# Kernel tuning notes

Measured on AMD Instinct MI355X. Metric: run time of the kernel, lower is better.

## Reference

```python
import jax, jax.numpy as jnp
import numpy as np
from jax import lax

C, NORI, NROT, K, PAD = 256, 8, 2, 3, 1
B, H, W = 16, 64, 64
EPS = 1e-5


def setup_inputs() -> dict:
    key = jax.random.key(0)
    k1, k2, k3 = jax.random.split(key, 3)
    x = jax.random.normal(k1, (B, C, H, W), dtype=jnp.float32)
    # rotate_arf() output: [nRot*C, nOri*C, K, K]
    weight_all = jax.random.normal(k2, (NROT * C, NORI * C, K, K), dtype=jnp.float32) * 0.02
    bias_all = jax.random.normal(k3, (NROT * C,), dtype=jnp.float32) * 0.02
    alpha = jnp.float32(1.0)
    gamma = jnp.ones((C,), dtype=jnp.float32)
    beta = jnp.zeros((C,), dtype=jnp.float32)
    return {"x": x, "weight_all": weight_all, "bias_all": bias_all,
            "alpha": alpha, "gamma": gamma, "beta": beta}


def _forward(x, weight_all, bias_all, alpha, gamma, beta):
    # Loop of nOri*nRot convs over the same x with different weight blocks,
    # all accumulated into one [B,C,H,W] tensor == single conv with summed blocks
    # (conv is linear in the weights): fused form of the original loop.
    W_eff = weight_all.reshape(NROT, C, NORI, C, K, K).sum(axis=(0, 2))  # [C, C, K, K]
    b_eff = bias_all.reshape(NROT, C).sum(axis=0) * NORI                 # [C]
    d_sum = lax.conv_general_dilated(
        x, W_eff, window_strides=(1, 1), padding=[(PAD, PAD), (PAD, PAD)],
        dimension_numbers=("NCHW", "OIHW", "NCHW"))
    d_sum = d_sum + b_eff[None, :, None, None]
    d_mean = d_sum / float(NORI * NROT)
    out = x + alpha * d_mean
    # BatchNorm2d, training mode: biased batch stats over (B, H, W)
    mean = out.mean(axis=(0, 2, 3))
    var = ((out - mean[None, :, None, None]) ** 2).mean(axis=(0, 2, 3))
    inv = lax.rsqrt(var + EPS)
    y = (out - mean[None, :, None, None]) * (gamma * inv)[None, :, None, None] \
        + beta[None, :, None, None]
    return y


def reference(x, weight_all, bias_all, alpha, gamma, beta):
    return _forward(x, weight_all, bias_all, alpha, gamma, beta)
```

## Files before the change

### kernel.cpp

```cpp
#include <hip/hip_runtime.h>
#include <stdint.h>

typedef __attribute__((__ext_vector_type__(8))) __bf16 bf16x8;
typedef __attribute__((__ext_vector_type__(4))) float  f32x4;

#define XT_OFF    0ul
#define WT_OFF    33554432ul
#define BEFF_OFF  34734080ul
#define ZERO_OFF  34737152ul
#define STATS_OFF 34737408ul
#define V_OFF     35651584ul
#define WS_NEED   (V_OFF + 33554432ul)

__device__ inline void gload_lds16(const void* g, void* l) {
  __builtin_amdgcn_global_load_lds((const __attribute__((address_space(1))) void*)g,
                                   (__attribute__((address_space(3))) void*)l,
                                   16, 0, 0);
}

__global__ void k_wred(const float* __restrict__ w, const float* __restrict__ bias,
                       const float* __restrict__ alpha_p, __bf16* __restrict__ Wt,
                       float* __restrict__ beff, float* __restrict__ zerob,
                       float* __restrict__ statsG) {
  const int co = blockIdx.x;
  const int ci = threadIdx.x;
  float a[9];
#pragma unroll
  for (int t = 0; t < 9; ++t) a[t] = 0.f;
#pragma unroll
  for (int r = 0; r < 2; ++r)
#pragma unroll
    for (int o = 0; o < 8; ++o) {
      const float* p = w + ((size_t)(r * 256 + co) * 2048 + (size_t)(o * 256 + ci)) * 9;
#pragma unroll
      for (int t = 0; t < 9; ++t) a[t] += p[t];
    }
  const float sc = alpha_p[0] * 0.0625f;
  const int s = ci >> 6, cis = ci & 63;
#pragma unroll
  for (int t = 0; t < 9; ++t)
    Wt[(size_t)(t * 4 + s) * 16384 + co * 64 + cis] = (__bf16)(a[t] * sc);
  if (ci == 0) beff[co] = (bias[co] + bias[256 + co]) * 8.0f * sc;
  if (blockIdx.x == 0) {
    statsG[ci] = 0.f; statsG[256 + ci] = 0.f;
    if (ci < 64) zerob[ci] = 0.f;
  }
}

__global__ void k_xpose(const float* __restrict__ x, __bf16* __restrict__ xT) {
  __shared__ __bf16 lds[64 * 258];
  int bh = blockIdx.x;
  int b = bh >> 6, h = bh & 63;
  int t = threadIdx.x;
  int w = t & 63, cg = t >> 6;
  const float* xb = x + ((size_t)b * 16384 + h) * 64;
#pragma unroll 4
  for (int cb = 0; cb < 256; cb += 4) {
    int ci = cb + cg;
    lds[w * 258 + ci] = (__bf16)xb[(size_t)ci * 4096 + w];
  }
  __syncthreads();
  const uint32_t* l32 = (const uint32_t*)lds;
  uint32_t* o32 = (uint32_t*)(xT + ((size_t)b * 64 + h) * 64 * 256);
  int c2 = t & 127, wg = t >> 7;
  for (int w0 = 0; w0 < 64; w0 += 2) {
    int ww = w0 + wg;
    o32[ww * 128 + c2] = l32[ww * 129 + c2];
  }
}

#define A_BYTES 51200
#define B_BYTES 32768

__global__ __launch_bounds__(1024) void k_conv(
    const float* __restrict__ x, const __bf16* __restrict__ xT,
    const __bf16* __restrict__ Wt, const float* __restrict__ beff,
    const __bf16* __restrict__ zerob, float* __restrict__ out,
    float* __restrict__ statsG, __bf16* __restrict__ vout, int use_v16)
{
  __shared__ __align__(16) char lds[A_BYTES + 3 * B_BYTES + 2048];
  const int bb   = blockIdx.x >> 4;
  const int ho0  = (blockIdx.x & 15) << 2;
  const int tid  = threadIdx.x;
  const int lane = tid & 63;
  const int wid  = tid >> 6;
  const int wr   = wid >> 2;
  const int wc   = wid & 3;
  const int l15  = lane & 15;

  f32x4 acc[4][4];
#pragma unroll
  for (int i = 0; i < 4; ++i)
#pragma unroll
    for (int j = 0; j < 4; ++j)
#pragma unroll
      for (int r = 0; r < 4; ++r) acc[i][j][r] = 0.f;

  const char* zb = (const char*)zerob;

  int boff[4][2];
#pragma unroll
  for (int j = 0; j < 4; ++j)
#pragma unroll
    for (int kk = 0; kk < 2; ++kk) {
      const int co     = (wc << 6) + (j << 4) + l15;
      const int ci_off = (kk << 5) + ((lane >> 4) << 3);
      boff[j][kk] = ((co << 7) + (ci_off << 1)) ^ ((co & 7) << 4);
    }
  const int bl = lane >> 3;
  const int bsrcLane = (bl << 7) + (((lane & 7) ^ (bl & 7)) << 4);

  auto stageA = [&](int s) {
    const int ci0 = s << 6;
    for (int t = wid; t < 50; t += 16) {
      const int ch = (t << 3) + (lane >> 3);
      const int r  = ch / 66;
      const int c  = ch - r * 66;
      const int ir = ho0 - 1 + r;
      const int ic = c - 1;
      const int k  = (lane & 7) ^ (ch & 7);
      const char* src;
      if (ch < 396 && ir >= 0 && ir < 64 && ic >= 0 && ic < 64)
        src = (const char*)(xT + ((((size_t)bb << 6) + ir) * 64 + ic) * 256 + ci0 + (k << 3));
      else
        src = zb + (k << 4);
      gload_lds16(src, lds + (t << 10));
    }
  };

  auto stageB = [&](int ph, int bi) {
    char* buf = lds + A_BYTES + bi * B_BYTES;
    const int s2 = ph / 9, tp = ph - s2 * 9;
    const char* wsrc = (const char*)Wt + ((size_t)(tp * 4 + s2) << 15) + bsrcLane;
    gload_lds16(wsrc + (wid << 10), buf + (wid << 10));
    gload_lds16(wsrc + ((wid + 16) << 10), buf + ((wid + 16) << 10));
  };

  stageA(0);
  stageB(0, 0);
  stageB(1, 1);
  asm volatile("s_waitcnt vmcnt(0)" ::: "memory");
  __builtin_amdgcn_s_barrier();
  asm volatile("" ::: "memory");

  int s = 0, tap = 0, bcur = 0;
  for (int p = 0; p < 36; ++p) {
    if (p + 2 < 36) {
      int bnx = bcur + 2; if (bnx >= 3) bnx -= 3;
      stageB(p + 2, bnx);
    }
    const int dh = (tap >= 6) ? 2 : (tap >= 3 ? 1 : 0);
    const int dw = tap - dh * 3;
    const char* Bb = lds + A_BYTES + bcur * B_BYTES;
    __builtin_amdgcn_s_setprio(1);
#pragma unroll
    for (int kk = 0; kk < 2; ++kk) {
      const int ci_off = (kk << 5) + ((lane >> 4) << 3);
      bf16x8 av[4];
#pragma unroll
      for (int i = 0; i < 4; ++i) {
        const int pos = (wr + dh) * 66 + (i << 4) + l15 + dw;
        const int off = ((pos << 7) + (ci_off << 1)) ^ ((pos & 7) << 4);
        av[i] = *(const bf16x8*)(lds + off);
      }
#pragma unroll
      for (int j = 0; j < 4; ++j) {
        const bf16x8 bv = *(const bf16x8*)(Bb + boff[j][kk]);
#pragma unroll
        for (int i = 0; i < 4; ++i)
          acc[i][j] = __builtin_amdgcn_mfma_f32_16x16x32_bf16(av[i], bv, acc[i][j], 0, 0, 0);
      }
    }
    __builtin_amdgcn_s_setprio(0);

    if (tap == 8 && s < 3) {
      asm volatile("s_waitcnt vmcnt(0)" ::: "memory");
      __builtin_amdgcn_s_barrier();
      asm volatile("" ::: "memory");
      stageA(s + 1);
      asm volatile("s_waitcnt vmcnt(0)" ::: "memory");
      __builtin_amdgcn_s_barrier();
      asm volatile("" ::: "memory");
    } else if (p + 2 < 36) {
      asm volatile("s_waitcnt vmcnt(2)" ::: "memory");
      __builtin_amdgcn_s_barrier();
      asm volatile("" ::: "memory");
    } else if (p < 35) {
      asm volatile("s_waitcnt vmcnt(0)" ::: "memory");
      __builtin_amdgcn_s_barrier();
      asm volatile("" ::: "memory");
    }
    if (++tap == 9) { tap = 0; ++s; }
    if (++bcur == 3) bcur = 0;
  }

  __syncthreads();
  float* lstat = (float*)(lds + A_BYTES + 3 * B_BYTES);
  if (tid < 512) lstat[tid] = 0.f;
  __syncthreads();

  const int wq = lane >> 4;
  const int ho = ho0 + wr;
#pragma unroll
  for (int j = 0; j < 4; ++j) {
    const int co = (wc << 6) + (j << 4) + l15;
    const float be = beff[co];
    const size_t base = ((((size_t)bb << 8) + (size_t)co) << 12) + (ho << 6);
    float r1 = 0.f, r2 = 0.f;
#pragma unroll
    for (int i = 0; i < 4; ++i) {
      const int w0 = (i << 4) + (wq << 2);
      const float4 xv = *(const float4*)(x + base + w0);
      float4 v;
      v.x = acc[i][j][0] + xv.x + be;
      v.y = acc[i][j][1] + xv.y + be;
      v.z = acc[i][j][2] + xv.z + be;
      v.w = acc[i][j][3] + xv.w + be;
      r1 += v.x + v.y + v.z + v.w;
      r2 += v.x * v.x + v.y * v.y + v.z * v.z + v.w * v.w;
      if (use_v16) {
        union { __bf16 h[4]; uint2 u2; } pk;
        pk.h[0] = (__bf16)v.x; pk.h[1] = (__bf16)v.y;
        pk.h[2] = (__bf16)v.z; pk.h[3] = (__bf16)v.w;
        *(uint2*)(vout + base + w0) = pk.u2;
      } else {
        *(float4*)(out + base + w0) = v;
      }
    }
    r1 += __shfl_xor(r1, 16); r2 += __shfl_xor(r2, 16);
    r1 += __shfl_xor(r1, 32); r2 += __shfl_xor(r2, 32);
    if (lane < 16) {
      atomicAdd(&lstat[co], r1);
      atomicAdd(&lstat[256 + co], r2);
    }
  }
  __syncthreads();
  if (tid < 512) atomicAdd(&statsG[tid], lstat[tid]);
}

__global__ void k_apply_v16(const __bf16* __restrict__ v, float* __restrict__ out,
                            const float* __restrict__ statsG,
                            const float* __restrict__ gamma,
                            const float* __restrict__ beta) {
  __shared__ float ssc[256], ssh[256];
  const int t = threadIdx.x;
  {
    const float mean = statsG[t] * (1.f / 65536.f);
    const float var  = statsG[256 + t] * (1.f / 65536.f) - mean * mean;
    const float inv  = rsqrtf(var + 1e-5f);
    const float sc   = gamma[t] * inv;
    ssc[t] = sc;
    ssh[t] = beta[t] - mean * sc;
  }
  __syncthreads();
  const ushort4* vp = (const ushort4*)v;
  float4* op = (float4*)out;
  for (size_t g = (size_t)blockIdx.x * 256 + t; g < 4194304ul; g += (size_t)gridDim.x * 256) {
    const int co = (int)((g >> 10) & 255);
    const ushort4 pv = vp[g];
    const float sc = ssc[co], sh = ssh[co];
    float4 y;
    y.x = __uint_as_float((uint32_t)pv.x << 16) * sc + sh;
    y.y = __uint_as_float((uint32_t)pv.y << 16) * sc + sh;
    y.z = __uint_as_float((uint32_t)pv.z << 16) * sc + sh;
    y.w = __uint_as_float((uint32_t)pv.w << 16) * sc + sh;
    op[g] = y;
  }
}

__global__ void k_apply_f32(float* __restrict__ out, const float* __restrict__ statsG,
                            const float* __restrict__ gamma,
                            const float* __restrict__ beta) {
  __shared__ float ssc[256], ssh[256];
  const int t = threadIdx.x;
  {
    const float mean = statsG[t] * (1.f / 65536.f);
    const float var  = statsG[256 + t] * (1.f / 65536.f) - mean * mean;
    const float inv  = rsqrtf(var + 1e-5f);
    const float sc   = gamma[t] * inv;
    ssc[t] = sc;
    ssh[t] = beta[t] - mean * sc;
  }
  __syncthreads();
  float4* op = (float4*)out;
  for (size_t g = (size_t)blockIdx.x * 256 + t; g < 4194304ul; g += (size_t)gridDim.x * 256) {
    const int co = (int)((g >> 10) & 255);
    float4 y = op[g];
    const float sc = ssc[co], sh = ssh[co];
    y.x = y.x * sc + sh; y.y = y.y * sc + sh;
    y.z = y.z * sc + sh; y.w = y.w * sc + sh;
    op[g] = y;
  }
}

extern "C" void kernel_launch(void* const* d_in, const int* in_sizes, int n_in,
                              void* d_out, int out_size, void* d_ws, size_t ws_size,
                              hipStream_t stream) {
  const float* x     = (const float*)d_in[0];
  const float* wall  = (const float*)d_in[1];
  const float* bias  = (const float*)d_in[2];
  const float* alpha = (const float*)d_in[3];
  const float* gamma = (const float*)d_in[4];
  const float* beta  = (const float*)d_in[5];
  float* out = (float*)d_out;

  char* ws = (char*)d_ws;
  __bf16* xT     = (__bf16*)(ws + XT_OFF);
  __bf16* Wt     = (__bf16*)(ws + WT_OFF);
  float*  beff   = (float*)(ws + BEFF_OFF);
  float*  zerob  = (float*)(ws + ZERO_OFF);
  float*  statsG = (float*)(ws + STATS_OFF);
  __bf16* vbuf   = (__bf16*)(ws + V_OFF);
  const int use_v16 = (ws_size >= WS_NEED) ? 1 : 0;

  k_wred<<<256, 256, 0, stream>>>(wall, bias, alpha, Wt, beff, zerob, statsG);
  k_xpose<<<1024, 256, 0, stream>>>(x, xT);
  k_conv<<<256, 1024, 0, stream>>>(x, xT, Wt, beff, (const __bf16*)zerob, out,
                                   statsG, vbuf, use_v16);
  if (use_v16)
    k_apply_v16<<<2048, 256, 0, stream>>>(vbuf, out, statsG, gamma, beta);
  else
    k_apply_f32<<<2048, 256, 0, stream>>>(out, statsG, gamma, beta);
}
```

Baseline: 126.7 us.

## Merge prep kernels, stage bf16 conv output through LDS for wide stores

Folds the weight-reduction and input-transpose kernels into one launch, with the block index choosing the role, which saves a kernel launch and lets the two jobs run concurrently. In the conv epilogue the bf16 intermediate is written to a per-wave swizzled LDS region and read back so each lane issues 16-byte global stores instead of 8-byte ones. The apply kernel now reads 16-byte vectors of eight bf16 values. This adds LDS traffic and waitcnt stalls in the epilogue, and the stats buffer is moved to offset 32768, which relies on the earlier LDS contents no longer being needed.

```diff
diff --git a/kernel.cpp b/kernel.cpp
--- a/kernel.cpp
+++ b/kernel.cpp
@@ -18,54 +18,55 @@
                                    16, 0, 0);
 }
 
-__global__ void k_wred(const float* __restrict__ w, const float* __restrict__ bias,
+__global__ void k_prep(const float* __restrict__ w, const float* __restrict__ bias,
                        const float* __restrict__ alpha_p, __bf16* __restrict__ Wt,
                        float* __restrict__ beff, float* __restrict__ zerob,
-                       float* __restrict__ statsG) {
-  const int co = blockIdx.x;
-  const int ci = threadIdx.x;
-  float a[9];
-#pragma unroll
-  for (int t = 0; t < 9; ++t) a[t] = 0.f;
-#pragma unroll
-  for (int r = 0; r < 2; ++r)
-#pragma unroll
-    for (int o = 0; o < 8; ++o) {
-      const float* p = w + ((size_t)(r * 256 + co) * 2048 + (size_t)(o * 256 + ci)) * 9;
-#pragma unroll
-      for (int t = 0; t < 9; ++t) a[t] += p[t];
-    }
-  const float sc = alpha_p[0] * 0.0625f;
-  const int s = ci >> 6, cis = ci & 63;
-#pragma unroll
-  for (int t = 0; t < 9; ++t)
-    Wt[(size_t)(t * 4 + s) * 16384 + co * 64 + cis] = (__bf16)(a[t] * sc);
-  if (ci == 0) beff[co] = (bias[co] + bias[256 + co]) * 8.0f * sc;
-  if (blockIdx.x == 0) {
-    statsG[ci] = 0.f; statsG[256 + ci] = 0.f;
-    if (ci < 64) zerob[ci] = 0.f;
-  }
-}
-
-__global__ void k_xpose(const float* __restrict__ x, __bf16* __restrict__ xT) {
+                       float* __restrict__ statsG,
+                       const float* __restrict__ x, __bf16* __restrict__ xT) {
   __shared__ __bf16 lds[64 * 258];
-  int bh = blockIdx.x;
-  int b = bh >> 6, h = bh & 63;
-  int t = threadIdx.x;
-  int w = t & 63, cg = t >> 6;
-  const float* xb = x + ((size_t)b * 16384 + h) * 64;
+  if (blockIdx.x < 256) {
+    const int co = blockIdx.x;
+    const int ci = threadIdx.x;
+    float a[9];
+#pragma unroll
+    for (int t = 0; t < 9; ++t) a[t] = 0.f;
+#pragma unroll
+    for (int r = 0; r < 2; ++r)
+#pragma unroll
+      for (int o = 0; o < 8; ++o) {
+        const float* p = w + ((size_t)(r * 256 + co) * 2048 + (size_t)(o * 256 + ci)) * 9;
+#pragma unroll
+        for (int t = 0; t < 9; ++t) a[t] += p[t];
+      }
+    const float sc = alpha_p[0] * 0.0625f;
+    const int s = ci >> 6, cis = ci & 63;
+#pragma unroll
+    for (int t = 0; t < 9; ++t)
+      Wt[(size_t)(t * 4 + s) * 16384 + co * 64 + cis] = (__bf16)(a[t] * sc);
+    if (ci == 0) beff[co] = (bias[co] + bias[256 + co]) * 8.0f * sc;
+    if (blockIdx.x == 0) {
+      statsG[ci] = 0.f; statsG[256 + ci] = 0.f;
+      if (ci < 64) zerob[ci] = 0.f;
+    }
+  } else {
+    int bh = blockIdx.x - 256;
+    int b = bh >> 6, h = bh & 63;
+    int t = threadIdx.x;
+    int w2 = t & 63, cg = t >> 6;
+    const float* xb = x + ((size_t)b * 16384 + h) * 64;
 #pragma unroll 4
-  for (int cb = 0; cb < 256; cb += 4) {
-    int ci = cb + cg;
-    lds[w * 258 + ci] = (__bf16)xb[(size_t)ci * 4096 + w];
-  }
-  __syncthreads();
-  const uint32_t* l32 = (const uint32_t*)lds;
-  uint32_t* o32 = (uint32_t*)(xT + ((size_t)b * 64 + h) * 64 * 256);
-  int c2 = t & 127, wg = t >> 7;
-  for (int w0 = 0; w0 < 64; w0 += 2) {
-    int ww = w0 + wg;
-    o32[ww * 128 + c2] = l32[ww * 129 + c2];
+    for (int cb = 0; cb < 256; cb += 4) {
+      int ci = cb + cg;
+      lds[w2 * 258 + ci] = (__bf16)xb[(size_t)ci * 4096 + w2];
+    }
+    __syncthreads();
+    const uint32_t* l32 = (const uint32_t*)lds;
+    uint32_t* o32 = (uint32_t*)(xT + ((size_t)b * 64 + h) * 64 * 256);
+    int c2 = t & 127, wg = t >> 7;
+    for (int w0 = 0; w0 < 64; w0 += 2) {
+      int ww = w0 + wg;
+      o32[ww * 128 + c2] = l32[ww * 129 + c2];
+    }
   }
 }
 
@@ -195,12 +196,14 @@
   }
 
   __syncthreads();
-  float* lstat = (float*)(lds + A_BYTES + 3 * B_BYTES);
+  float* lstat = (float*)(lds + 32768);
   if (tid < 512) lstat[tid] = 0.f;
   __syncthreads();
 
+  char* wreg = lds + wid * 2048;
   const int wq = lane >> 4;
   const int ho = ho0 + wr;
+  const int xorco = (l15 & 7) << 4;
 #pragma unroll
   for (int j = 0; j < 4; ++j) {
     const int co = (wc << 6) + (j << 4) + l15;
@@ -219,10 +222,11 @@
       r1 += v.x + v.y + v.z + v.w;
       r2 += v.x * v.x + v.y * v.y + v.z * v.z + v.w * v.w;
       if (use_v16) {
-        union { __bf16 h[4]; uint2 u2; } pk;
+        union { __bf16 h[4]; uint64_t u; } pk;
         pk.h[0] = (__bf16)v.x; pk.h[1] = (__bf16)v.y;
         pk.h[2] = (__bf16)v.z; pk.h[3] = (__bf16)v.w;
-        *(uint2*)(vout + base + w0) = pk.u2;
+        const int wa = (l15 << 7) + (i << 5) + (wq << 3);
+        *(uint64_t*)(wreg + (wa ^ xorco)) = pk.u;
       } else {
         *(float4*)(out + base + w0) = v;
       }
@@ -232,6 +236,20 @@
     if (lane < 16) {
       atomicAdd(&lstat[co], r1);
       atomicAdd(&lstat[256 + co], r2);
+    }
+    if (use_v16) {
+      asm volatile("s_waitcnt lgkmcnt(0)" ::: "memory");
+#pragma unroll
+      for (int t2 = 0; t2 < 2; ++t2) {
+        const int co_r = lane >> 2;
+        const int ch   = (lane & 3) + (t2 << 2);
+        const int ra   = (co_r << 7) + (ch << 4);
+        const uint4 pv = *(const uint4*)(wreg + (ra ^ ((co_r & 7) << 4)));
+        const int co_g = (wc << 6) + (j << 4) + co_r;
+        const size_t oi = ((((size_t)bb << 8) + (size_t)co_g) << 12) + (ho << 6) + (ch << 3);
+        *(uint4*)(vout + oi) = pv;
+      }
+      asm volatile("s_waitcnt lgkmcnt(0)" ::: "memory");
     }
   }
   __syncthreads();
@@ -253,18 +271,23 @@
     ssh[t] = beta[t] - mean * sc;
   }
   __syncthreads();
-  const ushort4* vp = (const ushort4*)v;
-  float4* op = (float4*)out;
-  for (size_t g = (size_t)blockIdx.x * 256 + t; g < 4194304ul; g += (size_t)gridDim.x * 256) {
-    const int co = (int)((g >> 10) & 255);
-    const ushort4 pv = vp[g];
+  const uint4* vp = (const uint4*)v;
+  for (size_t g = (size_t)blockIdx.x * 256 + t; g < 2097152ul; g += (size_t)gridDim.x * 256) {
+    const int co = (int)((g >> 9) & 255);
+    const uint4 pv = vp[g];
     const float sc = ssc[co], sh = ssh[co];
-    float4 y;
-    y.x = __uint_as_float((uint32_t)pv.x << 16) * sc + sh;
-    y.y = __uint_as_float((uint32_t)pv.y << 16) * sc + sh;
-    y.z = __uint_as_float((uint32_t)pv.z << 16) * sc + sh;
-    y.w = __uint_as_float((uint32_t)pv.w << 16) * sc + sh;
-    op[g] = y;
+    float4 y0, y1;
+    y0.x = __uint_as_float((pv.x & 0xffffu) << 16) * sc + sh;
+    y0.y = __uint_as_float(pv.x & 0xffff0000u) * sc + sh;
+    y0.z = __uint_as_float((pv.y & 0xffffu) << 16) * sc + sh;
+    y0.w = __uint_as_float(pv.y & 0xffff0000u) * sc + sh;
+    y1.x = __uint_as_float((pv.z & 0xffffu) << 16) * sc + sh;
+    y1.y = __uint_as_float(pv.z & 0xffff0000u) * sc + sh;
+    y1.z = __uint_as_float((pv.w & 0xffffu) << 16) * sc + sh;
+    y1.w = __uint_as_float(pv.w & 0xffff0000u) * sc + sh;
+    float4* op = (float4*)(out + g * 8);
+    op[0] = y0;
+    op[1] = y1;
   }
 }
 
@@ -313,8 +336,7 @@
   __bf16* vbuf   = (__bf16*)(ws + V_OFF);
   const int use_v16 = (ws_size >= WS_NEED) ? 1 : 0;
 
-  k_wred<<<256, 256, 0, stream>>>(wall, bias, alpha, Wt, beff, zerob, statsG);
-  k_xpose<<<1024, 256, 0, stream>>>(x, xT);
+  k_prep<<<1280, 256, 0, stream>>>(wall, bias, alpha, Wt, beff, zerob, statsG, x, xT);
   k_conv<<<256, 1024, 0, stream>>>(x, xT, Wt, beff, (const __bf16*)zerob, out,
                                    statsG, vbuf, use_v16);
   if (use_v16)
```

Result: faster. 122.7 us (-3.1%).
